# Performance work log

Hardware: AMD Instinct MI355X
Metric: run time of the kernel (lower is better)

Reference implementation:

```python
import jax, jax.numpy as jnp
import numpy as np

N, NFEAT, NHEADS, C = 4096, 512, 8, 64  # C = nhid = nclass (per-head dim)
NEG_INF = -9e15


def glorot(key, shape):
    fan = shape[-2] + shape[-1]
    stdv = np.sqrt(6.0 / fan)
    return jax.random.uniform(key, shape, jnp.float32, -stdv, stdv)


def setup_inputs() -> dict:
    key = jax.random.key(0)
    k_x, k_adj, k_w, k_al, k_ar = jax.random.split(key, 5)
    x = jax.random.normal(k_x, (N, NFEAT), jnp.float32)
    adj = jax.random.randint(k_adj, (N, N), 0, 2, jnp.int32)
    W = glorot(k_w, (NFEAT, NHEADS * C))          # linear weight (in, out)
    b = jnp.zeros((NHEADS * C,), jnp.float32)     # linear bias
    att_l = glorot(k_al, (NHEADS, C))
    att_r = glorot(k_ar, (NHEADS, C))
    return {"x": x, "adj": adj, "W": W, "b": b, "att_l": att_l, "att_r": att_r}


def reference(x, adj, W, b, att_l, att_r):
    # linear projection, viewed per-head: [N, H, C]
    x_l = (x @ W + b).reshape(N, NHEADS, C)
    # per-node scalar scores per head: [N, H]
    alpha_l = jnp.einsum('nhc,hc->nh', x_l, att_l)
    alpha_r = jnp.einsum('nhc,hc->nh', x_l, att_r)
    # outer-product scores [N_dst, N_src, H]  (== bmm + permute(1,2,0))
    scores = alpha_l[:, None, :] * alpha_r[None, :, :]
    # adjacency mask + softmax over source nodes (axis=1)
    scores = jnp.where(adj[:, :, None] > 0, scores, NEG_INF)
    att = jax.nn.softmax(scores, axis=1)          # [N, N, H]
    # aggregate neighbor features, ReLU, concat heads
    out = jnp.einsum('ijh,jhc->ihc', att, x_l)    # [N, H, C]
    return jax.nn.relu(out.reshape(N, NHEADS * C))
```

## Files before the change

### kernel.cpp

```cpp
#include <hip/hip_runtime.h>
#include <hip/hip_bf16.h>


#define NN    4096
#define NF    512
#define NH    8
#define CC    64
#define HC    512
#define GEMM_BLOCKS 512
#define PACK_BLOCKS 4096

typedef __bf16 bf16x8 __attribute__((ext_vector_type(8)));
typedef __bf16 bf16x4 __attribute__((ext_vector_type(4)));
typedef float  f32x4  __attribute__((ext_vector_type(4)));
typedef unsigned long long u64;

__device__ __forceinline__ float exp2_raw(float x) {
    float r;
    asm("v_exp_f32 %0, %1" : "=v"(r) : "v"(x));
    return r;
}

__global__ __launch_bounds__(256) void kA(
    const int* __restrict__ adj, u64* __restrict__ bits,
    const float* __restrict__ X, const float* __restrict__ W,
    const float* __restrict__ bias, const float* __restrict__ attl,
    const float* __restrict__ attr, __bf16* __restrict__ xlS,
    float* __restrict__ alT, float* __restrict__ arT)
{
    const int tid = threadIdx.x;

    if (blockIdx.x >= GEMM_BLOCKS) {
        const int bid = blockIdx.x - GEMM_BLOCKS;
        const int stride = PACK_BLOCKS * 256;
        for (int t = bid * 256 + tid; t < NN * NN; t += stride) {
            u64 m = __ballot(adj[t] != 0);
            if ((tid & 63) == 0) {
                const int i  = t >> 12;
                const int jw = (t & 4095) >> 6;
                bits[((i >> 5) * 64 + jw) * 32 + (i & 31)] = m;
            }
        }
        return;
    }

    __shared__ __bf16 As[64][40];
    __shared__ __bf16 BsT[64][40];
    __shared__ __bf16 T[64][72];

    const int w  = tid >> 6;
    const int l  = tid & 63;
    const int lo = l & 15;
    const int hi = l >> 4;
    const int r0 = (blockIdx.x & 63) * 64;
    const int h  = blockIdx.x >> 6;
    const int c0 = h * CC;
    const int wm = (w >> 1) * 32;
    const int wn = (w & 1) * 32;

    f32x4 acc[2][2];
#pragma unroll
    for (int m = 0; m < 2; ++m)
#pragma unroll
        for (int n = 0; n < 2; ++n) acc[m][n] = (f32x4){0.f, 0.f, 0.f, 0.f};

    const int arow = tid >> 3;
    const int acol = (tid & 7) * 4;
    const int brow = tid >> 4;
    const int bcol = (tid & 15) * 4;

    for (int k0 = 0; k0 < NF; k0 += 32) {
        __syncthreads();
#pragma unroll
        for (int p = 0; p < 2; ++p) {
            int r = arow + p * 32;
            float4 v = *reinterpret_cast<const float4*>(&X[(r0 + r) * NF + k0 + acol]);
            bf16x4 av;
            av[0] = (__bf16)v.x; av[1] = (__bf16)v.y; av[2] = (__bf16)v.z; av[3] = (__bf16)v.w;
            *reinterpret_cast<bf16x4*>(&As[r][acol]) = av;
        }
#pragma unroll
        for (int p = 0; p < 2; ++p) {
            int kk = brow + p * 16;
            float4 v = *reinterpret_cast<const float4*>(&W[(k0 + kk) * HC + c0 + bcol]);
            BsT[bcol + 0][kk] = (__bf16)v.x;
            BsT[bcol + 1][kk] = (__bf16)v.y;
            BsT[bcol + 2][kk] = (__bf16)v.z;
            BsT[bcol + 3][kk] = (__bf16)v.w;
        }
        __syncthreads();

        bf16x8 a[2], b[2];
#pragma unroll
        for (int m = 0; m < 2; ++m)
            a[m] = *reinterpret_cast<const bf16x8*>(&As[wm + m * 16 + lo][hi * 8]);
#pragma unroll
        for (int n = 0; n < 2; ++n)
            b[n] = *reinterpret_cast<const bf16x8*>(&BsT[wn + n * 16 + lo][hi * 8]);
#pragma unroll
        for (int m = 0; m < 2; ++m)
#pragma unroll
            for (int n = 0; n < 2; ++n)
                acc[m][n] = __builtin_amdgcn_mfma_f32_16x16x32_bf16(a[m], b[n], acc[m][n], 0, 0, 0);
    }

    __syncthreads();
#pragma unroll
    for (int n = 0; n < 2; ++n) {
        const float bv = bias[c0 + wn + n * 16 + lo];
#pragma unroll
        for (int m = 0; m < 2; ++m)
#pragma unroll
            for (int r = 0; r < 4; ++r)
                T[wm + m * 16 + hi * 4 + r][wn + n * 16 + lo] = (__bf16)(acc[m][n][r] + bv);
    }
    __syncthreads();

    {
        const int jw = blockIdx.x & 63;
#pragma unroll
        for (int p = 0; p < 2; ++p) {
            const int z   = tid + p * 256;
            const int s   = z >> 8;
            const int n   = (z >> 6) & 3;
            const int ln  = z & 63;
            const int hi2 = ln >> 4;
            const int lo2 = ln & 15;
            bf16x8 g;
#pragma unroll
            for (int e = 0; e < 8; ++e)
                g[e] = T[s * 32 + hi2 * 8 + e][n * 16 + lo2];
            *reinterpret_cast<bf16x8*>(
                &xlS[(size_t)((((h * 64 + jw) * 2 + s) * 4 + n) * 64 + ln) * 8]) = g;
        }
    }
    {
        const int row = tid >> 2;
        const int q   = tid & 3;
        float pl = 0.f, pr = 0.f;
#pragma unroll
        for (int c = 0; c < 16; ++c) {
            const int cc = q * 16 + c;
            const float f = (float)T[row][cc];
            pl += f * attl[c0 + cc];
            pr += f * attr[c0 + cc];
        }
        pl += __shfl_xor(pl, 1); pl += __shfl_xor(pl, 2);
        pr += __shfl_xor(pr, 1); pr += __shfl_xor(pr, 2);
        if (q == 0) {
            alT[h * NN + r0 + row] = pl * 1.4426950408889634f;
            arT[h * NN + r0 + row] = pr;
        }
    }
}

__global__ __launch_bounds__(512) void k3_attn(
    const u64* __restrict__ bitsT, const __bf16* __restrict__ xlS,
    const float* __restrict__ alT, const float* __restrict__ arT,
    float* __restrict__ out)
{
    __shared__ float rb[4][64][21];

    const int tid = threadIdx.x;
    const int wv  = tid >> 6;
    const int l   = tid & 63;
    const int lo  = l & 15;
    const int hi  = l >> 4;
    const int h   = blockIdx.x;
    const int i0  = blockIdx.y * 32;

    const float al20 = alT[h * NN + i0 + lo];
    const float al21 = alT[h * NN + i0 + 16 + lo];

    f32x4 acc[2][4];
    f32x4 accz[2];
#pragma unroll
    for (int m = 0; m < 2; ++m) {
        accz[m] = (f32x4){0.f, 0.f, 0.f, 0.f};
#pragma unroll
        for (int n = 0; n < 4; ++n) acc[m][n] = (f32x4){0.f, 0.f, 0.f, 0.f};
    }
    bf16x8 ones;
#pragma unroll
    for (int j = 0; j < 8; ++j) ones[j] = (__bf16)1.0f;

    const u64* bT = bitsT + (size_t)blockIdx.y * 64 * 32;
    const float* arp = &arT[h * NN];
    const __bf16* xs = xlS + (size_t)h * 64 * 4096;
    const int w0 = wv * 8;

#pragma unroll
    for (int it = 0; it < 8; ++it) {
        const int jw = w0 + it;
        const u64 ab0 = bT[jw * 32 + lo];
        const u64 ab1 = bT[jw * 32 + 16 + lo];
#pragma unroll
        for (int s = 0; s < 2; ++s) {
            const int jj = jw * 64 + s * 32 + hi * 8;
            const f32x4 rv0 = *reinterpret_cast<const f32x4*>(arp + jj);
            const f32x4 rv1 = *reinterpret_cast<const f32x4*>(arp + jj + 4);
            bf16x8 bX[4];
#pragma unroll
            for (int n = 0; n < 4; ++n)
                bX[n] = *reinterpret_cast<const bf16x8*>(
                    &xs[(size_t)(((jw * 2 + s) * 4 + n) * 64 + l) * 8]);
            const int sh = s * 32 + hi * 8;
#pragma unroll
            for (int m = 0; m < 2; ++m) {
                const unsigned int byte = (unsigned int)(((m ? ab1 : ab0) >> sh) & 0xffULL);
                const float alm = m ? al21 : al20;
                const float b0 = (byte & 1u)   ? 0.f : -1000.f;
                const float b1 = (byte & 2u)   ? 0.f : -1000.f;
                const float b2 = (byte & 4u)   ? 0.f : -1000.f;
                const float b3 = (byte & 8u)   ? 0.f : -1000.f;
                const float b4 = (byte & 16u)  ? 0.f : -1000.f;
                const float b5 = (byte & 32u)  ? 0.f : -1000.f;
                const float b6 = (byte & 64u)  ? 0.f : -1000.f;
                const float b7 = (byte & 128u) ? 0.f : -1000.f;
                const float p0 = exp2_raw(__builtin_fmaf(alm, rv0[0], b0));
                const float p1 = exp2_raw(__builtin_fmaf(alm, rv0[1], b1));
                const float p2 = exp2_raw(__builtin_fmaf(alm, rv0[2], b2));
                const float p3 = exp2_raw(__builtin_fmaf(alm, rv0[3], b3));
                const float p4 = exp2_raw(__builtin_fmaf(alm, rv1[0], b4));
                const float p5 = exp2_raw(__builtin_fmaf(alm, rv1[1], b5));
                const float p6 = exp2_raw(__builtin_fmaf(alm, rv1[2], b6));
                const float p7 = exp2_raw(__builtin_fmaf(alm, rv1[3], b7));
                bf16x8 aP;
                aP[0] = (__bf16)p0; aP[1] = (__bf16)p1; aP[2] = (__bf16)p2; aP[3] = (__bf16)p3;
                aP[4] = (__bf16)p4; aP[5] = (__bf16)p5; aP[6] = (__bf16)p6; aP[7] = (__bf16)p7;
                accz[m] = __builtin_amdgcn_mfma_f32_16x16x32_bf16(aP, ones, accz[m], 0, 0, 0);
#pragma unroll
                for (int n = 0; n < 4; ++n)
                    acc[m][n] = __builtin_amdgcn_mfma_f32_16x16x32_bf16(aP, bX[n], acc[m][n], 0, 0, 0);
            }
        }
    }

#pragma unroll
    for (int m = 0; m < 2; ++m) {
        if (wv >= 4) {
#pragma unroll
            for (int n = 0; n < 4; ++n)
#pragma unroll
                for (int r = 0; r < 4; ++r)
                    rb[wv - 4][l][n * 4 + r] = acc[m][n][r];
#pragma unroll
            for (int r = 0; r < 4; ++r)
                rb[wv - 4][l][16 + r] = accz[m][r];
        }
        __syncthreads();
        if (wv < 4) {
#pragma unroll
            for (int n = 0; n < 4; ++n)
#pragma unroll
                for (int r = 0; r < 4; ++r)
                    acc[m][n][r] += rb[wv][l][n * 4 + r];
#pragma unroll
            for (int r = 0; r < 4; ++r)
                accz[m][r] += rb[wv][l][16 + r];
        }
        __syncthreads();
        if (wv >= 2 && wv < 4) {
#pragma unroll
            for (int n = 0; n < 4; ++n)
#pragma unroll
                for (int r = 0; r < 4; ++r)
                    rb[wv - 2][l][n * 4 + r] = acc[m][n][r];
#pragma unroll
            for (int r = 0; r < 4; ++r)
                rb[wv - 2][l][16 + r] = accz[m][r];
        }
        __syncthreads();
        if (wv < 2) {
#pragma unroll
            for (int n = 0; n < 4; ++n)
#pragma unroll
                for (int r = 0; r < 4; ++r)
                    acc[m][n][r] += rb[wv][l][n * 4 + r];
#pragma unroll
            for (int r = 0; r < 4; ++r)
                accz[m][r] += rb[wv][l][16 + r];
        }
        __syncthreads();
        if (wv == 1) {
#pragma unroll
            for (int n = 0; n < 4; ++n)
#pragma unroll
                for (int r = 0; r < 4; ++r)
                    rb[0][l][n * 4 + r] = acc[m][n][r];
#pragma unroll
            for (int r = 0; r < 4; ++r)
                rb[0][l][16 + r] = accz[m][r];
        }
        __syncthreads();
        if (wv == 0) {
#pragma unroll
            for (int r = 0; r < 4; ++r) {
                const float zf = accz[m][r] + rb[0][l][16 + r];
                const float zr = __builtin_amdgcn_rcpf(zf);
                const int row = i0 + m * 16 + hi * 4 + r;
#pragma unroll
                for (int n = 0; n < 4; ++n) {
                    const float o = (acc[m][n][r] + rb[0][l][n * 4 + r]) * zr;
                    out[row * HC + h * CC + n * 16 + lo] = o > 0.f ? o : 0.f;
                }
            }
        }
        if (m == 0) __syncthreads();
    }
}

extern "C" void kernel_launch(void* const* d_in, const int* in_sizes, int n_in,
                              void* d_out, int out_size, void* d_ws, size_t ws_size,
                              hipStream_t stream)
{
    const float* x    = (const float*)d_in[0];
    const int*   adj  = (const int*)d_in[1];
    const float* W    = (const float*)d_in[2];
    const float* bias = (const float*)d_in[3];
    const float* attl = (const float*)d_in[4];
    const float* attr = (const float*)d_in[5];
    float* out = (float*)d_out;

    char* ws = (char*)d_ws;
    __bf16* xlS  = (__bf16*)(ws);
    float*  alT  = (float*)(ws + (4u << 20));
    float*  arT  = (float*)(ws + (4u << 20) + (128u << 10));
    u64*    abit = (u64*)(ws + (4u << 20) + (256u << 10));

    kA<<<dim3(GEMM_BLOCKS + PACK_BLOCKS), 256, 0, stream>>>(
        adj, abit, x, W, bias, attl, attr, xlS, alT, arT);
    k3_attn<<<dim3(NH, NN / 32), 512, 0, stream>>>(abit, xlS, alT, arT, out);
}
```

Baseline: 74.72 us.

## Pre-expand adjacency mask into bf16 AND-masks laid out in MFMA fragment order

The packing stage now expands the adjacency bits into 16-bit all-ones/zero masks, stored in the exact per-lane MFMA operand layout (32 MB buffer). The attention kernel loads these masks as vectors and ANDs them with the bf16 probabilities instead of decoding bits and adding a -1000 bias before each exp. This removes per-element bit extraction and select ALU work from the hot loop, at the cost of writing and reading 32x more mask bytes through memory. The old bit-packed path stays as a fallback when the workspace is too small.

```diff
diff --git a/kernel.cpp b/kernel.cpp
--- a/kernel.cpp
+++ b/kernel.cpp
@@ -13,6 +13,8 @@
 typedef __bf16 bf16x8 __attribute__((ext_vector_type(8)));
 typedef __bf16 bf16x4 __attribute__((ext_vector_type(4)));
 typedef float  f32x4  __attribute__((ext_vector_type(4)));
+typedef int    i32x4  __attribute__((ext_vector_type(4)));
+typedef unsigned int u32;
 typedef unsigned long long u64;
 
 __device__ __forceinline__ float exp2_raw(float x) {
@@ -21,8 +23,9 @@
     return r;
 }
 
+template<bool EXPAND>
 __global__ __launch_bounds__(256) void kA(
-    const int* __restrict__ adj, u64* __restrict__ bits,
+    const int* __restrict__ adj, void* __restrict__ maskout,
     const float* __restrict__ X, const float* __restrict__ W,
     const float* __restrict__ bias, const float* __restrict__ attl,
     const float* __restrict__ attr, __bf16* __restrict__ xlS,
@@ -31,14 +34,54 @@
     const int tid = threadIdx.x;
 
     if (blockIdx.x >= GEMM_BLOCKS) {
-        const int bid = blockIdx.x - GEMM_BLOCKS;
-        const int stride = PACK_BLOCKS * 256;
-        for (int t = bid * 256 + tid; t < NN * NN; t += stride) {
-            u64 m = __ballot(adj[t] != 0);
-            if ((tid & 63) == 0) {
-                const int i  = t >> 12;
-                const int jw = (t & 4095) >> 6;
-                bits[((i >> 5) * 64 + jw) * 32 + (i & 31)] = m;
+        const int bid  = blockIdx.x - GEMM_BLOCKS;
+        const int lane = tid & 63;
+        const int wid  = bid * 4 + (tid >> 6);
+
+        if (EXPAND) {
+            u32* mk = (u32*)maskout;
+            for (int u = wid; u < 32768; u += 16384) {
+                const int i0 = (u >> 6) * 8;
+                const int jw = u & 63;
+                const int ja = jw * 64 + lane;
+                const u64 b0 = __ballot(adj[(i0 + 0) * NN + ja] != 0);
+                const u64 b1 = __ballot(adj[(i0 + 1) * NN + ja] != 0);
+                const u64 b2 = __ballot(adj[(i0 + 2) * NN + ja] != 0);
+                const u64 b3 = __ballot(adj[(i0 + 3) * NN + ja] != 0);
+                const u64 b4 = __ballot(adj[(i0 + 4) * NN + ja] != 0);
+                const u64 b5 = __ballot(adj[(i0 + 5) * NN + ja] != 0);
+                const u64 b6 = __ballot(adj[(i0 + 6) * NN + ja] != 0);
+                const u64 b7 = __ballot(adj[(i0 + 7) * NN + ja] != 0);
+                const int r   = lane & 7;
+                const int shi = lane >> 3;
+                const u64 wr = (r < 4) ? ((r < 2) ? (r < 1 ? b0 : b1) : (r < 3 ? b2 : b3))
+                                       : ((r < 6) ? (r < 5 ? b4 : b5) : (r < 7 ? b6 : b7));
+                const u32 by = (u32)(wr >> (shi * 8)) & 0xffu;
+                const u32 d0 = ((by & 1u)   ? 0xFFFFu : 0u) | ((by & 2u)   ? 0xFFFF0000u : 0u);
+                const u32 d1 = ((by & 4u)   ? 0xFFFFu : 0u) | ((by & 8u)   ? 0xFFFF0000u : 0u);
+                const u32 d2 = ((by & 16u)  ? 0xFFFFu : 0u) | ((by & 32u)  ? 0xFFFF0000u : 0u);
+                const u32 d3 = ((by & 64u)  ? 0xFFFFu : 0u) | ((by & 128u) ? 0xFFFF0000u : 0u);
+                const int i     = i0 + r;
+                const int itile = i >> 5;
+                const int mr    = (i >> 4) & 1;
+                const int lo2   = i & 15;
+                const int s2    = shi >> 2;
+                const int hi2   = shi & 3;
+                const u32 offd = (u32)(itile * 64 + jw) * 1024u + (u32)s2 * 512u
+                               + (u32)mr * 256u + (u32)(hi2 * 16 + lo2) * 4u;
+                i32x4 dv = (i32x4){(int)d0, (int)d1, (int)d2, (int)d3};
+                *reinterpret_cast<i32x4*>(mk + offd) = dv;
+            }
+        } else {
+            u64* bits = (u64*)maskout;
+            const int stride = PACK_BLOCKS * 256;
+            for (int t = bid * 256 + tid; t < NN * NN; t += stride) {
+                u64 m = __ballot(adj[t] != 0);
+                if ((tid & 63) == 0) {
+                    const int i  = t >> 12;
+                    const int jw = (t & 4095) >> 6;
+                    bits[((i >> 5) * 64 + jw) * 32 + (i & 31)] = m;
+                }
             }
         }
         return;
@@ -154,8 +197,9 @@
     }
 }
 
+template<bool EXPAND>
 __global__ __launch_bounds__(512) void k3_attn(
-    const u64* __restrict__ bitsT, const __bf16* __restrict__ xlS,
+    const void* __restrict__ maskin, const __bf16* __restrict__ xlS,
     const float* __restrict__ alT, const float* __restrict__ arT,
     float* __restrict__ out)
 {
@@ -184,54 +228,98 @@
 #pragma unroll
     for (int j = 0; j < 8; ++j) ones[j] = (__bf16)1.0f;
 
-    const u64* bT = bitsT + (size_t)blockIdx.y * 64 * 32;
     const float* arp = &arT[h * NN];
-    const __bf16* xs = xlS + (size_t)h * 64 * 4096;
+    const __bf16* xs = xlS + (size_t)h * (64 * 4096);
     const int w0 = wv * 8;
 
-#pragma unroll
-    for (int it = 0; it < 8; ++it) {
-        const int jw = w0 + it;
-        const u64 ab0 = bT[jw * 32 + lo];
-        const u64 ab1 = bT[jw * 32 + 16 + lo];
-#pragma unroll
-        for (int s = 0; s < 2; ++s) {
-            const int jj = jw * 64 + s * 32 + hi * 8;
-            const f32x4 rv0 = *reinterpret_cast<const f32x4*>(arp + jj);
-            const f32x4 rv1 = *reinterpret_cast<const f32x4*>(arp + jj + 4);
-            bf16x8 bX[4];
-#pragma unroll
-            for (int n = 0; n < 4; ++n)
-                bX[n] = *reinterpret_cast<const bf16x8*>(
-                    &xs[(size_t)(((jw * 2 + s) * 4 + n) * 64 + l) * 8]);
-            const int sh = s * 32 + hi * 8;
-#pragma unroll
-            for (int m = 0; m < 2; ++m) {
-                const unsigned int byte = (unsigned int)(((m ? ab1 : ab0) >> sh) & 0xffULL);
-                const float alm = m ? al21 : al20;
-                const float b0 = (byte & 1u)   ? 0.f : -1000.f;
-                const float b1 = (byte & 2u)   ? 0.f : -1000.f;
-                const float b2 = (byte & 4u)   ? 0.f : -1000.f;
-                const float b3 = (byte & 8u)   ? 0.f : -1000.f;
-                const float b4 = (byte & 16u)  ? 0.f : -1000.f;
-                const float b5 = (byte & 32u)  ? 0.f : -1000.f;
-                const float b6 = (byte & 64u)  ? 0.f : -1000.f;
-                const float b7 = (byte & 128u) ? 0.f : -1000.f;
-                const float p0 = exp2_raw(__builtin_fmaf(alm, rv0[0], b0));
-                const float p1 = exp2_raw(__builtin_fmaf(alm, rv0[1], b1));
-                const float p2 = exp2_raw(__builtin_fmaf(alm, rv0[2], b2));
-                const float p3 = exp2_raw(__builtin_fmaf(alm, rv0[3], b3));
-                const float p4 = exp2_raw(__builtin_fmaf(alm, rv1[0], b4));
-                const float p5 = exp2_raw(__builtin_fmaf(alm, rv1[1], b5));
-                const float p6 = exp2_raw(__builtin_fmaf(alm, rv1[2], b6));
-                const float p7 = exp2_raw(__builtin_fmaf(alm, rv1[3], b7));
-                bf16x8 aP;
-                aP[0] = (__bf16)p0; aP[1] = (__bf16)p1; aP[2] = (__bf16)p2; aP[3] = (__bf16)p3;
-                aP[4] = (__bf16)p4; aP[5] = (__bf16)p5; aP[6] = (__bf16)p6; aP[7] = (__bf16)p7;
-                accz[m] = __builtin_amdgcn_mfma_f32_16x16x32_bf16(aP, ones, accz[m], 0, 0, 0);
+    if (EXPAND) {
+        const u32* mkb = (const u32*)maskin + (u32)blockIdx.y * 65536u;
+#pragma unroll
+        for (int it = 0; it < 8; ++it) {
+            const int jw = w0 + it;
+#pragma unroll
+            for (int s = 0; s < 2; ++s) {
+                const int jj = jw * 64 + s * 32 + hi * 8;
+                const f32x4 rv0 = *reinterpret_cast<const f32x4*>(arp + jj);
+                const f32x4 rv1 = *reinterpret_cast<const f32x4*>(arp + jj + 4);
+                bf16x8 bX[4];
 #pragma unroll
                 for (int n = 0; n < 4; ++n)
-                    acc[m][n] = __builtin_amdgcn_mfma_f32_16x16x32_bf16(aP, bX[n], acc[m][n], 0, 0, 0);
+                    bX[n] = *reinterpret_cast<const bf16x8*>(
+                        &xs[(jw * 2 + s) * 2048 + n * 512 + l * 8]);
+                const u32* mp = mkb + jw * 1024 + s * 512 + l * 4;
+                const i32x4 mk0 = *reinterpret_cast<const i32x4*>(mp);
+                const i32x4 mk1 = *reinterpret_cast<const i32x4*>(mp + 256);
+#pragma unroll
+                for (int m = 0; m < 2; ++m) {
+                    const float alm = m ? al21 : al20;
+                    const float p0 = exp2_raw(alm * rv0[0]);
+                    const float p1 = exp2_raw(alm * rv0[1]);
+                    const float p2 = exp2_raw(alm * rv0[2]);
+                    const float p3 = exp2_raw(alm * rv0[3]);
+                    const float p4 = exp2_raw(alm * rv1[0]);
+                    const float p5 = exp2_raw(alm * rv1[1]);
+                    const float p6 = exp2_raw(alm * rv1[2]);
+                    const float p7 = exp2_raw(alm * rv1[3]);
+                    bf16x8 aP;
+                    aP[0] = (__bf16)p0; aP[1] = (__bf16)p1; aP[2] = (__bf16)p2; aP[3] = (__bf16)p3;
+                    aP[4] = (__bf16)p4; aP[5] = (__bf16)p5; aP[6] = (__bf16)p6; aP[7] = (__bf16)p7;
+                    i32x4 ai = *reinterpret_cast<i32x4*>(&aP);
+                    ai &= (m ? mk1 : mk0);
+                    const bf16x8 aM = *reinterpret_cast<bf16x8*>(&ai);
+                    accz[m] = __builtin_amdgcn_mfma_f32_16x16x32_bf16(aM, ones, accz[m], 0, 0, 0);
+#pragma unroll
+                    for (int n = 0; n < 4; ++n)
+                        acc[m][n] = __builtin_amdgcn_mfma_f32_16x16x32_bf16(aM, bX[n], acc[m][n], 0, 0, 0);
+                }
+            }
+        }
+    } else {
+        const u64* bT = (const u64*)maskin + (size_t)blockIdx.y * 64 * 32;
+#pragma unroll
+        for (int it = 0; it < 8; ++it) {
+            const int jw = w0 + it;
+            const u64 ab0 = bT[jw * 32 + lo];
+            const u64 ab1 = bT[jw * 32 + 16 + lo];
+#pragma unroll
+            for (int s = 0; s < 2; ++s) {
+                const int jj = jw * 64 + s * 32 + hi * 8;
+                const f32x4 rv0 = *reinterpret_cast<const f32x4*>(arp + jj);
+                const f32x4 rv1 = *reinterpret_cast<const f32x4*>(arp + jj + 4);
+                bf16x8 bX[4];
+#pragma unroll
+                for (int n = 0; n < 4; ++n)
+                    bX[n] = *reinterpret_cast<const bf16x8*>(
+                        &xs[(jw * 2 + s) * 2048 + n * 512 + l * 8]);
+                const int sh = s * 32 + hi * 8;
+#pragma unroll
+                for (int m = 0; m < 2; ++m) {
+                    const u32 byte_ = (u32)(((m ? ab1 : ab0) >> sh) & 0xffULL);
+                    const float alm = m ? al21 : al20;
+                    const float b0 = (byte_ & 1u)   ? 0.f : -1000.f;
+                    const float b1 = (byte_ & 2u)   ? 0.f : -1000.f;
+                    const float b2 = (byte_ & 4u)   ? 0.f : -1000.f;
+                    const float b3 = (byte_ & 8u)   ? 0.f : -1000.f;
+                    const float b4 = (byte_ & 16u)  ? 0.f : -1000.f;
+                    const float b5 = (byte_ & 32u)  ? 0.f : -1000.f;
+                    const float b6 = (byte_ & 64u)  ? 0.f : -1000.f;
+                    const float b7 = (byte_ & 128u) ? 0.f : -1000.f;
+                    const float p0 = exp2_raw(__builtin_fmaf(alm, rv0[0], b0));
+                    const float p1 = exp2_raw(__builtin_fmaf(alm, rv0[1], b1));
+                    const float p2 = exp2_raw(__builtin_fmaf(alm, rv0[2], b2));
+                    const float p3 = exp2_raw(__builtin_fmaf(alm, rv0[3], b3));
+                    const float p4 = exp2_raw(__builtin_fmaf(alm, rv1[0], b4));
+                    const float p5 = exp2_raw(__builtin_fmaf(alm, rv1[1], b5));
+                    const float p6 = exp2_raw(__builtin_fmaf(alm, rv1[2], b6));
+                    const float p7 = exp2_raw(__builtin_fmaf(alm, rv1[3], b7));
+                    bf16x8 aP;
+                    aP[0] = (__bf16)p0; aP[1] = (__bf16)p1; aP[2] = (__bf16)p2; aP[3] = (__bf16)p3;
+                    aP[4] = (__bf16)p4; aP[5] = (__bf16)p5; aP[6] = (__bf16)p6; aP[7] = (__bf16)p7;
+                    accz[m] = __builtin_amdgcn_mfma_f32_16x16x32_bf16(aP, ones, accz[m], 0, 0, 0);
+#pragma unroll
+                    for (int n = 0; n < 4; ++n)
+                        acc[m][n] = __builtin_amdgcn_mfma_f32_16x16x32_bf16(aP, bX[n], acc[m][n], 0, 0, 0);
+                }
             }
         }
     }
@@ -323,12 +411,20 @@
     float* out = (float*)d_out;
 
     char* ws = (char*)d_ws;
-    __bf16* xlS  = (__bf16*)(ws);
-    float*  alT  = (float*)(ws + (4u << 20));
-    float*  arT  = (float*)(ws + (4u << 20) + (128u << 10));
-    u64*    abit = (u64*)(ws + (4u << 20) + (256u << 10));
-
-    kA<<<dim3(GEMM_BLOCKS + PACK_BLOCKS), 256, 0, stream>>>(
-        adj, abit, x, W, bias, attl, attr, xlS, alT, arT);
-    k3_attn<<<dim3(NH, NN / 32), 512, 0, stream>>>(abit, xlS, alT, arT, out);
+    __bf16* xlS = (__bf16*)(ws);
+    float*  alT = (float*)(ws + (4u << 20));
+    float*  arT = (float*)(ws + (4u << 20) + (128u << 10));
+    void*   msk = (void*)(ws + (4u << 20) + (256u << 10));
+
+    const size_t need_big = (4ull << 20) + (256ull << 10) + (32ull << 20);
+
+    if (ws_size >= need_big) {
+        kA<true><<<dim3(GEMM_BLOCKS + PACK_BLOCKS), 256, 0, stream>>>(
+            adj, msk, x, W, bias, attl, attr, xlS, alT, arT);
+        k3_attn<true><<<dim3(NH, NN / 32), 512, 0, stream>>>(msk, xlS, alT, arT, out);
+    } else {
+        kA<false><<<dim3(GEMM_BLOCKS + PACK_BLOCKS), 256, 0, stream>>>(
+            adj, msk, x, W, bias, attl, attr, xlS, alT, arT);
+        k3_attn<false><<<dim3(NH, NN / 32), 512, 0, stream>>>(msk, xlS, alT, arT, out);
+    }
 }
```

After: 74.00 us. No clear change (-1.0%).

## Widen attention row tile to 64 and batch adjacency bit-packing per wave

Applied to the files above, without the earlier changes.

The attention kernel now handles 64 destination rows per block instead of 32. Each wave loads its xl feature fragments once and reuses them across four row groups, which halves the grid size and the redundant xl/arT loads. The adjacency packer now has each wave pack eight rows per iteration with eight independent ballots, giving more memory-level parallelism than the old one-row-per-iteration grid-stride loop. In exchange, the accumulator register count doubles, which may lower occupancy or cause spills, and the cross-wave reduction runs four times per block.

```diff
diff --git a/kernel.cpp b/kernel.cpp
--- a/kernel.cpp
+++ b/kernel.cpp
@@ -13,6 +13,7 @@
 typedef __bf16 bf16x8 __attribute__((ext_vector_type(8)));
 typedef __bf16 bf16x4 __attribute__((ext_vector_type(4)));
 typedef float  f32x4  __attribute__((ext_vector_type(4)));
+typedef unsigned int u32;
 typedef unsigned long long u64;
 
 __device__ __forceinline__ float exp2_raw(float x) {
@@ -31,14 +32,27 @@
     const int tid = threadIdx.x;
 
     if (blockIdx.x >= GEMM_BLOCKS) {
-        const int bid = blockIdx.x - GEMM_BLOCKS;
-        const int stride = PACK_BLOCKS * 256;
-        for (int t = bid * 256 + tid; t < NN * NN; t += stride) {
-            u64 m = __ballot(adj[t] != 0);
-            if ((tid & 63) == 0) {
-                const int i  = t >> 12;
-                const int jw = (t & 4095) >> 6;
-                bits[((i >> 5) * 64 + jw) * 32 + (i & 31)] = m;
+        const int bid  = blockIdx.x - GEMM_BLOCKS;
+        const int lane = tid & 63;
+        const int wid  = bid * 4 + (tid >> 6);
+        for (int u = wid; u < 32768; u += 16384) {
+            const int i0 = (u >> 6) * 8;
+            const int jw = u & 63;
+            const int ja = jw * 64 + lane;
+            const u64 b0 = __ballot(adj[(i0 + 0) * NN + ja] != 0);
+            const u64 b1 = __ballot(adj[(i0 + 1) * NN + ja] != 0);
+            const u64 b2 = __ballot(adj[(i0 + 2) * NN + ja] != 0);
+            const u64 b3 = __ballot(adj[(i0 + 3) * NN + ja] != 0);
+            const u64 b4 = __ballot(adj[(i0 + 4) * NN + ja] != 0);
+            const u64 b5 = __ballot(adj[(i0 + 5) * NN + ja] != 0);
+            const u64 b6 = __ballot(adj[(i0 + 6) * NN + ja] != 0);
+            const u64 b7 = __ballot(adj[(i0 + 7) * NN + ja] != 0);
+            if (lane < 8) {
+                const int r = lane;
+                const u64 wr = (r < 4) ? ((r < 2) ? (r < 1 ? b0 : b1) : (r < 3 ? b2 : b3))
+                                       : ((r < 6) ? (r < 5 ? b4 : b5) : (r < 7 ? b6 : b7));
+                const int i = i0 + r;
+                bits[((i >> 5) * 64 + jw) * 32 + (i & 31)] = wr;
             }
         }
         return;
@@ -155,7 +169,7 @@
 }
 
 __global__ __launch_bounds__(512) void k3_attn(
-    const u64* __restrict__ bitsT, const __bf16* __restrict__ xlS,
+    const u64* __restrict__ bits, const __bf16* __restrict__ xlS,
     const float* __restrict__ alT, const float* __restrict__ arT,
     float* __restrict__ out)
 {
@@ -167,33 +181,37 @@
     const int lo  = l & 15;
     const int hi  = l >> 4;
     const int h   = blockIdx.x;
-    const int i0  = blockIdx.y * 32;
-
-    const float al20 = alT[h * NN + i0 + lo];
-    const float al21 = alT[h * NN + i0 + 16 + lo];
-
-    f32x4 acc[2][4];
-    f32x4 accz[2];
-#pragma unroll
-    for (int m = 0; m < 2; ++m) {
-        accz[m] = (f32x4){0.f, 0.f, 0.f, 0.f};
-#pragma unroll
-        for (int n = 0; n < 4; ++n) acc[m][n] = (f32x4){0.f, 0.f, 0.f, 0.f};
+    const int by  = blockIdx.y;
+    const int i0  = by * 64;
+
+    float al2[4];
+#pragma unroll
+    for (int g = 0; g < 4; ++g) al2[g] = alT[h * NN + i0 + g * 16 + lo];
+
+    f32x4 acc[4][4];
+    f32x4 accz[4];
+#pragma unroll
+    for (int g = 0; g < 4; ++g) {
+        accz[g] = (f32x4){0.f, 0.f, 0.f, 0.f};
+#pragma unroll
+        for (int n = 0; n < 4; ++n) acc[g][n] = (f32x4){0.f, 0.f, 0.f, 0.f};
     }
     bf16x8 ones;
 #pragma unroll
     for (int j = 0; j < 8; ++j) ones[j] = (__bf16)1.0f;
 
-    const u64* bT = bitsT + (size_t)blockIdx.y * 64 * 32;
     const float* arp = &arT[h * NN];
-    const __bf16* xs = xlS + (size_t)h * 64 * 4096;
+    const __bf16* xs = xlS + (size_t)h * (64 * 4096);
+    const u64* bbase = bits + (size_t)(by * 2) * 64 * 32;
     const int w0 = wv * 8;
 
 #pragma unroll
     for (int it = 0; it < 8; ++it) {
         const int jw = w0 + it;
-        const u64 ab0 = bT[jw * 32 + lo];
-        const u64 ab1 = bT[jw * 32 + 16 + lo];
+        u64 ab[4];
+#pragma unroll
+        for (int g = 0; g < 4; ++g)
+            ab[g] = bbase[((g >> 1) * 64 + jw) * 32 + (g & 1) * 16 + lo];
 #pragma unroll
         for (int s = 0; s < 2; ++s) {
             const int jj = jw * 64 + s * 32 + hi * 8;
@@ -203,20 +221,20 @@
 #pragma unroll
             for (int n = 0; n < 4; ++n)
                 bX[n] = *reinterpret_cast<const bf16x8*>(
-                    &xs[(size_t)(((jw * 2 + s) * 4 + n) * 64 + l) * 8]);
+                    &xs[(jw * 2 + s) * 2048 + n * 512 + l * 8]);
             const int sh = s * 32 + hi * 8;
 #pragma unroll
-            for (int m = 0; m < 2; ++m) {
-                const unsigned int byte = (unsigned int)(((m ? ab1 : ab0) >> sh) & 0xffULL);
-                const float alm = m ? al21 : al20;
-                const float b0 = (byte & 1u)   ? 0.f : -1000.f;
-                const float b1 = (byte & 2u)   ? 0.f : -1000.f;
-                const float b2 = (byte & 4u)   ? 0.f : -1000.f;
-                const float b3 = (byte & 8u)   ? 0.f : -1000.f;
-                const float b4 = (byte & 16u)  ? 0.f : -1000.f;
-                const float b5 = (byte & 32u)  ? 0.f : -1000.f;
-                const float b6 = (byte & 64u)  ? 0.f : -1000.f;
-                const float b7 = (byte & 128u) ? 0.f : -1000.f;
+            for (int g = 0; g < 4; ++g) {
+                const u32 byte_ = (u32)((ab[g] >> sh) & 0xffULL);
+                const float alm = al2[g];
+                const float b0 = (byte_ & 1u)   ? 0.f : -1000.f;
+                const float b1 = (byte_ & 2u)   ? 0.f : -1000.f;
+                const float b2 = (byte_ & 4u)   ? 0.f : -1000.f;
+                const float b3 = (byte_ & 8u)   ? 0.f : -1000.f;
+                const float b4 = (byte_ & 16u)  ? 0.f : -1000.f;
+                const float b5 = (byte_ & 32u)  ? 0.f : -1000.f;
+                const float b6 = (byte_ & 64u)  ? 0.f : -1000.f;
+                const float b7 = (byte_ & 128u) ? 0.f : -1000.f;
                 const float p0 = exp2_raw(__builtin_fmaf(alm, rv0[0], b0));
                 const float p1 = exp2_raw(__builtin_fmaf(alm, rv0[1], b1));
                 const float p2 = exp2_raw(__builtin_fmaf(alm, rv0[2], b2));
@@ -228,25 +246,25 @@
                 bf16x8 aP;
                 aP[0] = (__bf16)p0; aP[1] = (__bf16)p1; aP[2] = (__bf16)p2; aP[3] = (__bf16)p3;
                 aP[4] = (__bf16)p4; aP[5] = (__bf16)p5; aP[6] = (__bf16)p6; aP[7] = (__bf16)p7;
-                accz[m] = __builtin_amdgcn_mfma_f32_16x16x32_bf16(aP, ones, accz[m], 0, 0, 0);
+                accz[g] = __builtin_amdgcn_mfma_f32_16x16x32_bf16(aP, ones, accz[g], 0, 0, 0);
 #pragma unroll
                 for (int n = 0; n < 4; ++n)
-                    acc[m][n] = __builtin_amdgcn_mfma_f32_16x16x32_bf16(aP, bX[n], acc[m][n], 0, 0, 0);
+                    acc[g][n] = __builtin_amdgcn_mfma_f32_16x16x32_bf16(aP, bX[n], acc[g][n], 0, 0, 0);
             }
         }
     }
 
 #pragma unroll
-    for (int m = 0; m < 2; ++m) {
+    for (int g = 0; g < 4; ++g) {
         if (wv >= 4) {
 #pragma unroll
             for (int n = 0; n < 4; ++n)
 #pragma unroll
                 for (int r = 0; r < 4; ++r)
-                    rb[wv - 4][l][n * 4 + r] = acc[m][n][r];
-#pragma unroll
-            for (int r = 0; r < 4; ++r)
-                rb[wv - 4][l][16 + r] = accz[m][r];
+                    rb[wv - 4][l][n * 4 + r] = acc[g][n][r];
+#pragma unroll
+            for (int r = 0; r < 4; ++r)
+                rb[wv - 4][l][16 + r] = accz[g][r];
         }
         __syncthreads();
         if (wv < 4) {
@@ -254,10 +272,10 @@
             for (int n = 0; n < 4; ++n)
 #pragma unroll
                 for (int r = 0; r < 4; ++r)
-                    acc[m][n][r] += rb[wv][l][n * 4 + r];
-#pragma unroll
-            for (int r = 0; r < 4; ++r)
-                accz[m][r] += rb[wv][l][16 + r];
+                    acc[g][n][r] += rb[wv][l][n * 4 + r];
+#pragma unroll
+            for (int r = 0; r < 4; ++r)
+                accz[g][r] += rb[wv][l][16 + r];
         }
         __syncthreads();
         if (wv >= 2 && wv < 4) {
@@ -265,10 +283,10 @@
             for (int n = 0; n < 4; ++n)
 #pragma unroll
                 for (int r = 0; r < 4; ++r)
-                    rb[wv - 2][l][n * 4 + r] = acc[m][n][r];
-#pragma unroll
-            for (int r = 0; r < 4; ++r)
-                rb[wv - 2][l][16 + r] = accz[m][r];
+                    rb[wv - 2][l][n * 4 + r] = acc[g][n][r];
+#pragma unroll
+            for (int r = 0; r < 4; ++r)
+                rb[wv - 2][l][16 + r] = accz[g][r];
         }
         __syncthreads();
         if (wv < 2) {
@@ -276,10 +294,10 @@
             for (int n = 0; n < 4; ++n)
 #pragma unroll
                 for (int r = 0; r < 4; ++r)
-                    acc[m][n][r] += rb[wv][l][n * 4 + r];
-#pragma unroll
-            for (int r = 0; r < 4; ++r)
-                accz[m][r] += rb[wv][l][16 + r];
+                    acc[g][n][r] += rb[wv][l][n * 4 + r];
+#pragma unroll
+            for (int r = 0; r < 4; ++r)
+                accz[g][r] += rb[wv][l][16 + r];
         }
         __syncthreads();
         if (wv == 1) {
@@ -287,26 +305,26 @@
             for (int n = 0; n < 4; ++n)
 #pragma unroll
                 for (int r = 0; r < 4; ++r)
-                    rb[0][l][n * 4 + r] = acc[m][n][r];
-#pragma unroll
-            for (int r = 0; r < 4; ++r)
-                rb[0][l][16 + r] = accz[m][r];
+                    rb[0][l][n * 4 + r] = acc[g][n][r];
+#pragma unroll
+            for (int r = 0; r < 4; ++r)
+                rb[0][l][16 + r] = accz[g][r];
         }
         __syncthreads();
         if (wv == 0) {
 #pragma unroll
             for (int r = 0; r < 4; ++r) {
-                const float zf = accz[m][r] + rb[0][l][16 + r];
+                const float zf = accz[g][r] + rb[0][l][16 + r];
                 const float zr = __builtin_amdgcn_rcpf(zf);
-                const int row = i0 + m * 16 + hi * 4 + r;
+                const int row = i0 + g * 16 + hi * 4 + r;
 #pragma unroll
                 for (int n = 0; n < 4; ++n) {
-                    const float o = (acc[m][n][r] + rb[0][l][n * 4 + r]) * zr;
+                    const float o = (acc[g][n][r] + rb[0][l][n * 4 + r]) * zr;
                     out[row * HC + h * CC + n * 16 + lo] = o > 0.f ? o : 0.f;
                 }
             }
         }
-        if (m == 0) __syncthreads();
+        if (g < 3) __syncthreads();
     }
 }
 
@@ -330,5 +348,5 @@
 
     kA<<<dim3(GEMM_BLOCKS + PACK_BLOCKS), 256, 0, stream>>>(
         adj, abit, x, W, bias, attl, attr, xlS, alT, arT);
-    k3_attn<<<dim3(NH, NN / 32), 512, 0, stream>>>(abit, xlS, alT, arT, out);
+    k3_attn<<<dim3(NH, NN / 64), 512, 0, stream>>>(abit, xlS, alT, arT, out);
 }
```

New measurement: 70.61 us. 1.06x faster.
